# Kernel tuning notes

Measured on AMD Instinct MI355X. Metric: run time of the kernel, lower is better.

Reference implementation:

```python
import jax, jax.numpy as jnp
import numpy as np
from jax import lax

C_IN = 768      # in_channels == out_channels (required by routing_weight.view)
C_OUT = 768
E = 3           # num_experts
K = 3           # kernel_size
S = max(C_IN // 16, 16)  # squeeze_channels = 48
H = W = 120     # divisible by 3 and 5 -> adaptive pools are exact block means


def _bicubic_mat(in_size, out_size):
    """PyTorch-style bicubic (a=-0.75), align_corners=False, border-replicate."""
    a = -0.75
    def k(x):
        x = abs(x)
        if x <= 1.0:
            return (a + 2) * x**3 - (a + 3) * x**2 + 1.0
        if x < 2.0:
            return a * x**3 - 5 * a * x**2 + 8 * a * x - 4 * a
        return 0.0
    M = np.zeros((out_size, in_size), dtype=np.float32)
    scale = in_size / out_size
    for j in range(out_size):
        src = (j + 0.5) * scale - 0.5
        i0 = int(np.floor(src))
        t = src - i0
        for m in range(-1, 3):
            idx = min(max(i0 + m, 0), in_size - 1)
            M[j, idx] += k(m - t)
    return M

_M35 = jnp.asarray(_bicubic_mat(3, 5))  # (5, 3) separable interp matrix
_DN = ('NCHW', 'OIHW', 'NCHW')


def _route(x, w_pw1, w_dw1, w_dw2, w_pw2):
    b, c, h, w = x.shape
    a1 = x.mean(axis=(2, 3), keepdims=True)                       # (b,C,1,1)
    a3 = x.reshape(b, c, 3, h // 3, 3, w // 3).mean(axis=(3, 5))  # (b,C,3,3)
    a5 = x.reshape(b, c, 5, h // 5, 5, w // 5).mean(axis=(3, 5))  # (b,C,5,5)
    a3u = jnp.einsum('pi,bcij,qj->bcpq', _M35, a3, _M35)          # bicubic 3->5
    a1e = jnp.broadcast_to(a1, a5.shape)
    att = jnp.concatenate([a1e, a3u, a5], axis=1)                 # (b,3C,5,5)
    hdd = jax.nn.relu(jnp.einsum('oc,bchw->bohw', w_pw1, att))    # 1x1 conv -> (b,S,5,5)
    hdd = jax.nn.relu(lax.conv_general_dilated(hdd, w_dw1, (1, 1), 'VALID',
                                               dimension_numbers=_DN,
                                               feature_group_count=S))  # (b,S,3,3)
    hdd = jax.nn.relu(lax.conv_general_dilated(hdd, w_dw2, (1, 1), 'VALID',
                                               dimension_numbers=_DN,
                                               feature_group_count=S))  # (b,S,1,1)
    out = jnp.einsum('os,bshw->bohw', w_pw2, hdd)                 # (b,E*C,1,1)
    return jax.nn.sigmoid(out)


def setup_inputs() -> dict:
    key = jax.random.key(0)
    ks = jax.random.split(key, 6)
    return {
        'x':      jax.random.normal(ks[0], (1, C_IN, H, W), dtype=jnp.float32),
        'convs':  jax.random.normal(ks[1], (E, C_OUT, C_IN, K, K), dtype=jnp.float32) * 0.02,
        'w_pw1':  jax.random.normal(ks[2], (S, 3 * C_IN), dtype=jnp.float32) * 0.05,
        'w_dw1':  jax.random.normal(ks[3], (S, 1, 3, 3), dtype=jnp.float32) * 0.1,
        'w_dw2':  jax.random.normal(ks[4], (S, 1, 3, 3), dtype=jnp.float32) * 0.1,
        'w_pw2':  jax.random.normal(ks[5], (E * C_IN, S), dtype=jnp.float32) * 0.05,
    }


def reference(x, convs, w_pw1, w_dw1, w_dw2, w_pw2):
    # batch=1 inference path (DyResConv_Inf is only valid for b=1)
    r = _route(x, w_pw1, w_dw1, w_dw2, w_pw2)      # (1, E*C_OUT, 1, 1)
    r = r.reshape(E, C_OUT)                        # per-expert, per-out-channel gate
    w = jnp.einsum('eo,eoikl->oikl', r, convs)     # fused weight synthesis
    y = lax.conv_general_dilated(x, w, (1, 1), [(1, 1), (1, 1)],
                                 dimension_numbers=_DN)  # stride=1, pad=1
    return y
```

## Files before the change

### kernel.cpp

```cpp
#include <hip/hip_runtime.h>
#include <hip/hip_bf16.h>
#include <cstdint>
#include <cstddef>

#define C_IN 768
#define HW 120
#define WP 122
#define PIX (HW*HW)
#define PPIX (WP*WP)
#define S_CH 48
#define CCH 256
#define LSTR 257

#define OFF_POOL 0
#define OFF_HDD3 163840
#define OFF_WT   262144
#define OFF_XTP  10878976

typedef __attribute__((ext_vector_type(8))) short short8;
typedef __attribute__((ext_vector_type(4))) float floatx4;
typedef __attribute__((ext_vector_type(4))) uint uint4v;

#define AS3(p) ((__attribute__((address_space(3))) uint*)(p))
#define AS1(p) ((const __attribute__((address_space(1))) uint*)(p))

__device__ inline ushort f2bf(float f) {
  union { float f; uint i; } v; v.f = f;
  uint r = v.i + 0x7FFF + ((v.i >> 16) & 1);
  return (ushort)(r >> 16);
}

__device__ __constant__ float M35[5][3] = {
  { 1.096f, -0.096f,  0.000f },
  { 0.612f,  0.460f, -0.072f },
  { 0.000f,  1.000f,  0.000f },
  {-0.072f,  0.460f,  0.612f },
  { 0.000f, -0.096f,  1.096f },
};

__global__ __launch_bounds__(256) void k_pad_transpose(const float* __restrict__ x,
                                                       ushort* __restrict__ xTp) {
  int ph = blockIdx.x;
  int c0 = blockIdx.y * CCH;
  int tid = threadIdx.x;
  ushort* rowbase = xTp + (size_t)ph * WP * C_IN;
  if (ph == 0 || ph == WP - 1) {
    uint4v z = {0, 0, 0, 0};
    for (int i = tid; i < WP * (CCH / 8); i += 256) {
      int w = i / (CCH / 8), j = i % (CCH / 8);
      *(uint4v*)&rowbase[(size_t)w * C_IN + c0 + j * 8] = z;
    }
    return;
  }
  int h = ph - 1;
  __shared__ ushort T[HW * LSTR];
  int wave = tid >> 6, lane = tid & 63;
  for (int k = 0; k < 64; k++) {
    int cl = wave * 64 + k;
    const float* src = x + (size_t)(c0 + cl) * PIX + h * HW;
    if (lane < 60) {
      float vx = src[2 * lane], vy = src[2 * lane + 1];
      T[(2 * lane) * LSTR + cl]     = f2bf(vx);
      T[(2 * lane + 1) * LSTR + cl] = f2bf(vy);
    }
  }
  __syncthreads();
  if (tid < 128) {
    *(uint*)&rowbase[c0 + 2 * tid] = 0;
    *(uint*)&rowbase[(size_t)(WP - 1) * C_IN + c0 + 2 * tid] = 0;
  }
  for (int idx = tid; idx < HW * (CCH / 2); idx += 256) {
    int w = idx >> 7, pr = idx & 127;
    uint a = T[w * LSTR + 2 * pr];
    uint b = T[w * LSTR + 2 * pr + 1];
    *(uint*)&rowbase[(size_t)(1 + w) * C_IN + c0 + 2 * pr] = a | (b << 16);
  }
}

__global__ __launch_bounds__(256) void k_pool(const float* __restrict__ x,
                                              float* __restrict__ pooled) {
  int c = blockIdx.x;
  int tid = threadIdx.x;
  __shared__ float fine[225];
  __shared__ float s3[9], a3v[9], a5v[25];
  if (tid < 225) {
    int fr = tid / 15, fc = tid % 15;
    const float* base = x + (size_t)c * PIX + fr * 8 * HW + fc * 8;
    float s = 0.f;
#pragma unroll
    for (int r = 0; r < 8; r++) {
      floatx4 a = *(const floatx4*)(base + r * HW);
      floatx4 b = *(const floatx4*)(base + r * HW + 4);
#pragma unroll
      for (int j = 0; j < 4; j++) s += a[j] + b[j];
    }
    fine[tid] = s;
  }
  __syncthreads();
  if (tid < 9) {
    int i = tid / 3, j = tid % 3;
    float s = 0.f;
    for (int a = 0; a < 5; a++) for (int b = 0; b < 5; b++) s += fine[(i*5+a)*15 + j*5+b];
    s3[tid] = s; a3v[tid] = s / 1600.f;
  } else if (tid >= 32 && tid < 57) {
    int t = tid - 32; int p = t / 5, q = t % 5;
    float s = 0.f;
    for (int a = 0; a < 3; a++) for (int b = 0; b < 3; b++) s += fine[(p*3+a)*15 + q*3+b];
    a5v[t] = s / 576.f;
  }
  __syncthreads();
  float* out = pooled + c * 51;
  if (tid == 63) {
    float tot = 0.f;
    for (int k = 0; k < 9; k++) tot += s3[k];
    out[0] = tot / 14400.f;
  }
  if (tid < 25) {
    int p = tid / 5, q = tid % 5;
    float s = 0.f;
    for (int i = 0; i < 3; i++) for (int j = 0; j < 3; j++)
      s += M35[p][i] * M35[q][j] * a3v[i*3+j];
    out[1 + tid] = s;
    out[26 + tid] = a5v[tid];
  }
}

__global__ __launch_bounds__(256) void k_route(const float* __restrict__ pooled,
                                               const float* __restrict__ w_pw1,
                                               const float* __restrict__ w_dw1,
                                               const float* __restrict__ w_dw2,
                                               float* __restrict__ hdd3) {
  int s = blockIdx.x;
  int tid = threadIdx.x;
  __shared__ float red[26][256];
  float acc[25]; float accw1 = 0.f;
#pragma unroll
  for (int q = 0; q < 25; q++) acc[q] = 0.f;
  for (int c = tid; c < C_IN; c += 256) {
    const float* pl = pooled + c * 51;
    float w1 = w_pw1[(size_t)s * 3 * C_IN + c];
    float w2 = w_pw1[(size_t)s * 3 * C_IN + C_IN + c];
    float w3 = w_pw1[(size_t)s * 3 * C_IN + 2 * C_IN + c];
    accw1 += w1 * pl[0];
#pragma unroll
    for (int q = 0; q < 25; q++) acc[q] += w2 * pl[1 + q] + w3 * pl[26 + q];
  }
#pragma unroll
  for (int q = 0; q < 25; q++) red[q][tid] = acc[q];
  red[25][tid] = accw1;
  for (int st = 128; st; st >>= 1) {
    __syncthreads();
    if (tid < st)
      for (int q = 0; q < 26; q++) red[q][tid] += red[q][tid + st];
  }
  __syncthreads();
  if (tid == 0) {
    float hdd[5][5];
    for (int p = 0; p < 5; p++) for (int q = 0; q < 5; q++) {
      float v = red[p*5+q][0] + red[25][0];
      hdd[p][q] = v > 0.f ? v : 0.f;
    }
    float wd1[9], wd2[9];
    for (int i = 0; i < 9; i++) { wd1[i] = w_dw1[s*9 + i]; wd2[i] = w_dw2[s*9 + i]; }
    float h2[3][3];
    for (int i = 0; i < 3; i++) for (int j = 0; j < 3; j++) {
      float v = 0.f;
      for (int u = 0; u < 3; u++) for (int vv = 0; vv < 3; vv++) v += wd1[u*3+vv] * hdd[i+u][j+vv];
      h2[i][j] = v > 0.f ? v : 0.f;
    }
    float v = 0.f;
    for (int u = 0; u < 3; u++) for (int vv = 0; vv < 3; vv++) v += wd2[u*3+vv] * h2[u][vv];
    hdd3[s] = v > 0.f ? v : 0.f;
  }
}

__global__ __launch_bounds__(256) void k_wt(const float* __restrict__ convs,
                                            const float* __restrict__ w_pw2,
                                            const float* __restrict__ hdd3,
                                            ushort* __restrict__ wt) {
  int o = blockIdx.x;
  int tid = threadIdx.x;
  __shared__ float g[3];
  __shared__ __align__(16) ushort st[9 * C_IN];
  if (tid < 3) {
    float v = 0.f;
    for (int s = 0; s < S_CH; s++)
      v += w_pw2[((size_t)tid * C_IN + o) * S_CH + s] * hdd3[s];
    g[tid] = 1.f / (1.f + __expf(-v));
  }
  __syncthreads();
  float g0 = g[0], g1 = g[1], g2 = g[2];
  const float* c0p = convs + (size_t)o * 6912;
  const float* c1p = convs + (size_t)(C_IN + o) * 6912;
  const float* c2p = convs + (size_t)(2 * C_IN + o) * 6912;
  for (int i = tid * 4; i < 6912; i += 1024) {
    floatx4 a = *(const floatx4*)(c0p + i);
    floatx4 b = *(const floatx4*)(c1p + i);
    floatx4 c = *(const floatx4*)(c2p + i);
#pragma unroll
    for (int j = 0; j < 4; j++) {
      int idx = i + j;
      int cch = idx / 9, tap = idx - cch * 9;
      st[tap * C_IN + cch] = f2bf(g0 * a[j] + g1 * b[j] + g2 * c[j]);
    }
  }
  __syncthreads();
  for (int i = tid; i < 864; i += 256) {
    int tap = i / 96, j = i - tap * 96;
    *(uint4v*)&wt[((size_t)(tap * C_IN + o)) * C_IN + j * 8] =
        *(const uint4v*)&st[tap * C_IN + j * 8];
  }
}

__global__ __launch_bounds__(128) void k_conv(const ushort* __restrict__ xTp,
                                              const ushort* __restrict__ wt,
                                              float* __restrict__ y) {
  __shared__ __align__(16) ushort Aun[2][768 * 8];
  __shared__ __align__(16) ushort Bt[2][256 * 8];
  int tid = threadIdx.x;
  int lane = tid & 63;
  int quad = lane >> 4, l15 = lane & 15;
  int wave = tid >> 6;

  int bid = blockIdx.x;
  int wg = (bid & 7) * 180 + (bid >> 3);
  int n_t = wg / 120, m_t = wg - n_t * 120;
  int h0 = (m_t >> 3) << 3;
  int w0 = (m_t & 7) << 4;
  int n0 = n_t << 6;

  uint a_off[6];
#pragma unroll
  for (int r = 0; r < 6; r++) {
    int t = r * 128 + tid;
    int p = t >> 2; if (p > 179) p = 179;
    int sl = (t & 3) ^ ((p >> 1) & 3);
    int pr = p / 18, pc = p - pr * 18;
    int pix = (h0 + pr) * WP + (w0 + pc);
    if (pix > PPIX - 1) pix = PPIX - 1;
    a_off[r] = (uint)pix * C_IN + sl * 8;
  }
  uint b_off[2];
#pragma unroll
  for (int r = 0; r < 2; r++) {
    int t = r * 128 + tid;
    int n = t >> 2;
    int sl = (t & 3) ^ ((n >> 1) & 3);
    b_off[r] = (uint)(n0 + n) * C_IN + sl * 8;
  }
  int b_rd[4];
#pragma unroll
  for (int nt = 0; nt < 4; nt++) {
    int n = nt * 16 + l15;
    b_rd[nt] = n * 32 + ((quad ^ ((n >> 1) & 3)) << 3);
  }
  int amh = wave * 4;
  int P0[4];
#pragma unroll
  for (int mt = 0; mt < 4; mt++) P0[mt] = (amh + mt) * 18 + l15;

  auto stageA = [&](int ncc, int na) {
#pragma unroll
    for (int r = 0; r < 6; r++)
      __builtin_amdgcn_global_load_lds(AS1(xTp + a_off[r] + ncc * 32),
                                       AS3(&Aun[na][(r * 128 + wave * 64) * 8]), 16, 0, 0);
  };
  auto stageB = [&](int ncc, int ntap, int nb) {
    const ushort* wb = wt + (size_t)ntap * C_IN * C_IN + ncc * 32;
#pragma unroll
    for (int r = 0; r < 2; r++)
      __builtin_amdgcn_global_load_lds(AS1(wb + b_off[r]),
                                       AS3(&Bt[nb][(r * 128 + wave * 64) * 8]), 16, 0, 0);
  };

  floatx4 acc[4][4];
#pragma unroll
  for (int i = 0; i < 4; i++)
#pragma unroll
    for (int j = 0; j < 4; j++) acc[i][j] = (floatx4){0.f, 0.f, 0.f, 0.f};

  stageA(0, 0);
  stageB(0, 0, 0);
  __syncthreads();

  int pb = 0;
  for (int cc = 0; cc < 24; cc++) {
    int pa = cc & 1;
#pragma unroll
    for (int tap = 0; tap < 9; tap++) {
      const int kh = tap / 3, kw = tap % 3;
      if (tap < 8) {
        stageB(cc, tap + 1, pb ^ 1);
      } else if (cc < 23) {
        stageB(cc + 1, 0, pb ^ 1);
        stageA(cc + 1, pa ^ 1);
      }
      short8 bfr[4], af[4];
#pragma unroll
      for (int nt = 0; nt < 4; nt++) bfr[nt] = *(const short8*)&Bt[pb][b_rd[nt]];
#pragma unroll
      for (int mt = 0; mt < 4; mt++) {
        int p = P0[mt] + kh * 18 + kw;
        int idx = p * 32 + ((quad ^ ((p >> 1) & 3)) << 3);
        af[mt] = *(const short8*)&Aun[pa][idx];
      }
#pragma unroll
      for (int mt = 0; mt < 4; mt++)
#pragma unroll
        for (int nt = 0; nt < 4; nt++)
          acc[mt][nt] = __builtin_amdgcn_mfma_f32_16x16x32_bf16(af[mt], bfr[nt], acc[mt][nt], 0, 0, 0);
      __syncthreads();
      pb ^= 1;
    }
  }

#pragma unroll
  for (int mt = 0; mt < 4; mt++) {
    int h = h0 + wave * 4 + mt;
    int wbase = w0 + quad * 4;
    if (wbase < HW) {
#pragma unroll
      for (int nt = 0; nt < 4; nt++) {
        int n = n0 + nt * 16 + l15;
        *(floatx4*)&y[(size_t)n * PIX + h * HW + wbase] = acc[mt][nt];
      }
    }
  }
}

extern "C" void kernel_launch(void* const* d_in, const int* in_sizes, int n_in,
                              void* d_out, int out_size, void* d_ws, size_t ws_size,
                              hipStream_t stream) {
  const float* x     = (const float*)d_in[0];
  const float* convs = (const float*)d_in[1];
  const float* w_pw1 = (const float*)d_in[2];
  const float* w_dw1 = (const float*)d_in[3];
  const float* w_dw2 = (const float*)d_in[4];
  const float* w_pw2 = (const float*)d_in[5];
  float* y = (float*)d_out;
  char* ws = (char*)d_ws;
  float*  pooled = (float*)(ws + OFF_POOL);
  float*  hdd3   = (float*)(ws + OFF_HDD3);
  ushort* wt     = (ushort*)(ws + OFF_WT);
  ushort* xTp    = (ushort*)(ws + OFF_XTP);

  hipLaunchKernelGGL(k_pad_transpose, dim3(122, 3), dim3(256), 0, stream, x, xTp);
  hipLaunchKernelGGL(k_pool,          dim3(768),    dim3(256), 0, stream, x, pooled);
  hipLaunchKernelGGL(k_route,         dim3(48),     dim3(256), 0, stream, pooled, w_pw1, w_dw1, w_dw2, hdd3);
  hipLaunchKernelGGL(k_wt,            dim3(768),    dim3(256), 0, stream, convs, w_pw2, hdd3, wt);
  hipLaunchKernelGGL(k_conv,          dim3(1440),   dim3(128), 0, stream, xTp, wt, y);
}
```

Baseline: 410.9 us.

## Enlarge conv tile to 192x256 with 8 waves and 4-slot B pipeline

The implicit-GEMM conv kernel moves from 128-thread blocks with 128x64 tiles to 512-thread blocks covering 12 rows by 16 columns and 256 output channels, split over 8 waves in a 2x4 arrangement. The K-step doubles to 64 channels and is split into two 32-wide halves. B tiles rotate through four LDS slots and A is double-buffered, with explicit vmcnt waits, raw s_barrier and setprio around the MFMA blocks. The larger tile raises weight and activation reuse per byte loaded and lowers barrier overhead. In exchange it uses much more LDS and registers, and only 240 blocks are launched, which may leave some CUs idle.

New measurement: 329.2 us. 1.25x faster.

```diff
diff --git a/kernel.cpp b/kernel.cpp
--- a/kernel.cpp
+++ b/kernel.cpp
@@ -212,116 +212,166 @@
   }
 }
 
-__global__ __launch_bounds__(128) void k_conv(const ushort* __restrict__ xTp,
-                                              const ushort* __restrict__ wt,
-                                              float* __restrict__ y) {
-  __shared__ __align__(16) ushort Aun[2][768 * 8];
-  __shared__ __align__(16) ushort Bt[2][256 * 8];
+#define WAITV(N) asm volatile("s_waitcnt vmcnt(" #N ")" ::: "memory")
+#define FENCE()  asm volatile("" ::: "memory")
+
+#define PHASE(WSTMT, KS, RSLOT, PAv, KH, KW, STAGES) do {                      \
+    WSTMT;                                                                     \
+    short8 bfr[4], af[6];                                                      \
+    _Pragma("unroll")                                                          \
+    for (int nt = 0; nt < 4; nt++)                                             \
+      bfr[nt] = *(const short8*)&Bt[RSLOT][b_rd[nt]];                          \
+    _Pragma("unroll")                                                          \
+    for (int mt = 0; mt < 6; mt++) {                                           \
+      int u_ = P0[mt] + ((KH) * 18 + (KW));                                    \
+      int idx_ = u_ * 32 + ((quad ^ ((u_ >> 1) & 3)) << 3);                    \
+      af[mt] = *(const short8*)&Aun[PAv][KS][idx_];                            \
+    }                                                                          \
+    STAGES;                                                                    \
+    FENCE();                                                                   \
+    __builtin_amdgcn_s_barrier();                                              \
+    __builtin_amdgcn_sched_barrier(0);                                         \
+    __builtin_amdgcn_s_setprio(1);                                             \
+    _Pragma("unroll")                                                          \
+    for (int mt = 0; mt < 6; mt++)                                             \
+      _Pragma("unroll")                                                        \
+      for (int nt = 0; nt < 4; nt++)                                           \
+        acc[mt][nt] = __builtin_amdgcn_mfma_f32_16x16x32_bf16(af[mt], bfr[nt], \
+                                                              acc[mt][nt], 0, 0, 0); \
+    __builtin_amdgcn_s_setprio(0);                                             \
+  } while (0)
+
+#define CCB(ccv, P, PAv) do { const int cc_ = (ccv);                               \
+    PHASE(;,        0, ((0+P)&3),  PAv, 0,0, { SB(1, cc_, 1, ((3+P)&3)); });        \
+    PHASE(WAITV(0), 1, ((1+P)&3),  PAv, 0,0, { SB(2, cc_, 0, ((0+P)&3)); });        \
+    PHASE(;,        0, ((2+P)&3),  PAv, 0,1, { SB(2, cc_, 1, ((5+P)&3)); });        \
+    PHASE(WAITV(0), 1, ((3+P)&3),  PAv, 0,1, { SB(3, cc_, 0, ((2+P)&3)); });        \
+    PHASE(;,        0, ((4+P)&3),  PAv, 0,2, { SB(3, cc_, 1, ((7+P)&3)); });        \
+    PHASE(WAITV(0), 1, ((5+P)&3),  PAv, 0,2, { SB(4, cc_, 0, ((4+P)&3)); });        \
+    PHASE(;,        0, ((6+P)&3),  PAv, 1,0, { SB(4, cc_, 1, ((9+P)&3)); });        \
+    PHASE(WAITV(0), 1, ((7+P)&3),  PAv, 1,0, { SB(5, cc_, 0, ((6+P)&3)); });        \
+    PHASE(;,        0, ((8+P)&3),  PAv, 1,1, { SB(5, cc_, 1, ((11+P)&3)); SA(cc_+1, (PAv)^1, 0); }); \
+    PHASE(WAITV(1), 1, ((9+P)&3),  PAv, 1,1, { SB(6, cc_, 0, ((8+P)&3));  SA(cc_+1, (PAv)^1, 1); }); \
+    PHASE(;,        0, ((10+P)&3), PAv, 1,2, { SB(6, cc_, 1, ((13+P)&3)); SA(cc_+1, (PAv)^1, 2); }); \
+    PHASE(WAITV(1), 1, ((11+P)&3), PAv, 1,2, { SB(7, cc_, 0, ((10+P)&3)); SA(cc_+1, (PAv)^1, 3); }); \
+    PHASE(;,        0, ((12+P)&3), PAv, 2,0, { SB(7, cc_, 1, ((15+P)&3)); });       \
+    PHASE(WAITV(0), 1, ((13+P)&3), PAv, 2,0, { SB(8, cc_, 0, ((12+P)&3)); });       \
+    PHASE(;,        0, ((14+P)&3), PAv, 2,1, { SB(8, cc_, 1, ((17+P)&3)); });       \
+    PHASE(WAITV(0), 1, ((15+P)&3), PAv, 2,1, { SB(0, cc_+1, 0, ((14+P)&3)); });     \
+    PHASE(;,        0, ((16+P)&3), PAv, 2,2, { SB(0, cc_+1, 1, ((19+P)&3)); });     \
+    PHASE(WAITV(0), 1, ((17+P)&3), PAv, 2,2, { SB(1, cc_+1, 0, ((16+P)&3)); });     \
+  } while (0)
+
+#define CCB11() do { const int cc_ = 11;                                           \
+    PHASE(;,        0, ((0+2)&3),  1, 0,0, { SB(1, cc_, 1, ((3+2)&3)); });          \
+    PHASE(WAITV(0), 1, ((1+2)&3),  1, 0,0, { SB(2, cc_, 0, ((0+2)&3)); });          \
+    PHASE(;,        0, ((2+2)&3),  1, 0,1, { SB(2, cc_, 1, ((5+2)&3)); });          \
+    PHASE(WAITV(0), 1, ((3+2)&3),  1, 0,1, { SB(3, cc_, 0, ((2+2)&3)); });          \
+    PHASE(;,        0, ((4+2)&3),  1, 0,2, { SB(3, cc_, 1, ((7+2)&3)); });          \
+    PHASE(WAITV(0), 1, ((5+2)&3),  1, 0,2, { SB(4, cc_, 0, ((4+2)&3)); });          \
+    PHASE(;,        0, ((6+2)&3),  1, 1,0, { SB(4, cc_, 1, ((9+2)&3)); });          \
+    PHASE(WAITV(0), 1, ((7+2)&3),  1, 1,0, { SB(5, cc_, 0, ((6+2)&3)); });          \
+    PHASE(;,        0, ((8+2)&3),  1, 1,1, { SB(5, cc_, 1, ((11+2)&3)); });         \
+    PHASE(WAITV(0), 1, ((9+2)&3),  1, 1,1, { SB(6, cc_, 0, ((8+2)&3)); });          \
+    PHASE(;,        0, ((10+2)&3), 1, 1,2, { SB(6, cc_, 1, ((13+2)&3)); });         \
+    PHASE(WAITV(0), 1, ((11+2)&3), 1, 1,2, { SB(7, cc_, 0, ((10+2)&3)); });         \
+    PHASE(;,        0, ((12+2)&3), 1, 2,0, { SB(7, cc_, 1, ((15+2)&3)); });         \
+    PHASE(WAITV(0), 1, ((13+2)&3), 1, 2,0, { SB(8, cc_, 0, ((12+2)&3)); });         \
+    PHASE(;,        0, ((14+2)&3), 1, 2,1, { SB(8, cc_, 1, ((17+2)&3)); });         \
+    PHASE(WAITV(0), 1, ((15+2)&3), 1, 2,1, { ; });                                  \
+    PHASE(;,        0, ((16+2)&3), 1, 2,2, { ; });                                  \
+    PHASE(;,        1, ((17+2)&3), 1, 2,2, { ; });                                  \
+  } while (0)
+
+__global__ __launch_bounds__(512, 2) void k_conv(const ushort* __restrict__ xTp,
+                                                 const ushort* __restrict__ wt,
+                                                 float* __restrict__ y) {
+  __shared__ __align__(16) ushort Aun[2][2][8192];
+  __shared__ __align__(16) ushort Bt[4][8192];
   int tid = threadIdx.x;
   int lane = tid & 63;
   int quad = lane >> 4, l15 = lane & 15;
   int wave = tid >> 6;
+  int wm = wave >> 2, wn = wave & 3;
 
   int bid = blockIdx.x;
-  int wg = (bid & 7) * 180 + (bid >> 3);
-  int n_t = wg / 120, m_t = wg - n_t * 120;
-  int h0 = (m_t >> 3) << 3;
+  int wg = (bid & 7) * 30 + (bid >> 3);
+  int n_t = wg / 80, m_t = wg - n_t * 80;
+  int h0 = (m_t >> 3) * 12;
   int w0 = (m_t & 7) << 4;
-  int n0 = n_t << 6;
-
-  uint a_off[6];
-#pragma unroll
-  for (int r = 0; r < 6; r++) {
-    int t = r * 128 + tid;
-    int p = t >> 2; if (p > 179) p = 179;
-    int sl = (t & 3) ^ ((p >> 1) & 3);
-    int pr = p / 18, pc = p - pr * 18;
-    int pix = (h0 + pr) * WP + (w0 + pc);
+  int n0 = n_t << 8;
+
+  size_t a_off[4];
+#pragma unroll
+  for (int r = 0; r < 4; r++) {
+    int t = r * 512 + tid;
+    int ks = t >> 10;
+    int u = (t >> 2) & 255; if (u > 251) u = 251;
+    int sl = (t & 3) ^ ((u >> 1) & 3);
+    int ur = u / 18, uc = u - ur * 18;
+    int pix = (h0 + ur) * WP + (w0 + uc);
     if (pix > PPIX - 1) pix = PPIX - 1;
-    a_off[r] = (uint)pix * C_IN + sl * 8;
-  }
-  uint b_off[2];
+    a_off[r] = (size_t)pix * C_IN + ks * 32 + sl * 8;
+  }
+  size_t b_off[2];
 #pragma unroll
   for (int r = 0; r < 2; r++) {
-    int t = r * 128 + tid;
+    int t = r * 512 + tid;
     int n = t >> 2;
     int sl = (t & 3) ^ ((n >> 1) & 3);
-    b_off[r] = (uint)(n0 + n) * C_IN + sl * 8;
+    b_off[r] = (size_t)(n0 + n) * C_IN + sl * 8;
   }
   int b_rd[4];
 #pragma unroll
   for (int nt = 0; nt < 4; nt++) {
-    int n = nt * 16 + l15;
+    int n = wn * 64 + nt * 16 + l15;
     b_rd[nt] = n * 32 + ((quad ^ ((n >> 1) & 3)) << 3);
   }
-  int amh = wave * 4;
-  int P0[4];
-#pragma unroll
-  for (int mt = 0; mt < 4; mt++) P0[mt] = (amh + mt) * 18 + l15;
-
-  auto stageA = [&](int ncc, int na) {
-#pragma unroll
-    for (int r = 0; r < 6; r++)
-      __builtin_amdgcn_global_load_lds(AS1(xTp + a_off[r] + ncc * 32),
-                                       AS3(&Aun[na][(r * 128 + wave * 64) * 8]), 16, 0, 0);
+  int P0[6];
+#pragma unroll
+  for (int mt = 0; mt < 6; mt++) P0[mt] = (wm * 6 + mt) * 18 + l15;
+
+  auto SB = [&](int gtap, int gcc, int ks, int slot) {
+    const ushort* src = wt + (size_t)gtap * (C_IN * C_IN) + gcc * 64 + ks * 32;
+#pragma unroll
+    for (int r = 0; r < 2; r++)
+      __builtin_amdgcn_global_load_lds(AS1(src + b_off[r]),
+                                       AS3(&Bt[slot][r * 4096 + wave * 512]), 16, 0, 0);
   };
-  auto stageB = [&](int ncc, int ntap, int nb) {
-    const ushort* wb = wt + (size_t)ntap * C_IN * C_IN + ncc * 32;
-#pragma unroll
-    for (int r = 0; r < 2; r++)
-      __builtin_amdgcn_global_load_lds(AS1(wb + b_off[r]),
-                                       AS3(&Bt[nb][(r * 128 + wave * 64) * 8]), 16, 0, 0);
+  auto SA = [&](int gcc, int pa, int r) {
+    __builtin_amdgcn_global_load_lds(AS1(xTp + a_off[r] + gcc * 64),
+                                     AS3(&Aun[pa][0][0] + r * 4096 + wave * 512), 16, 0, 0);
   };
 
-  floatx4 acc[4][4];
-#pragma unroll
-  for (int i = 0; i < 4; i++)
+  floatx4 acc[6][4];
+#pragma unroll
+  for (int i = 0; i < 6; i++)
 #pragma unroll
     for (int j = 0; j < 4; j++) acc[i][j] = (floatx4){0.f, 0.f, 0.f, 0.f};
 
-  stageA(0, 0);
-  stageB(0, 0, 0);
-  __syncthreads();
-
-  int pb = 0;
-  for (int cc = 0; cc < 24; cc++) {
-    int pa = cc & 1;
-#pragma unroll
-    for (int tap = 0; tap < 9; tap++) {
-      const int kh = tap / 3, kw = tap % 3;
-      if (tap < 8) {
-        stageB(cc, tap + 1, pb ^ 1);
-      } else if (cc < 23) {
-        stageB(cc + 1, 0, pb ^ 1);
-        stageA(cc + 1, pa ^ 1);
-      }
-      short8 bfr[4], af[4];
-#pragma unroll
-      for (int nt = 0; nt < 4; nt++) bfr[nt] = *(const short8*)&Bt[pb][b_rd[nt]];
-#pragma unroll
-      for (int mt = 0; mt < 4; mt++) {
-        int p = P0[mt] + kh * 18 + kw;
-        int idx = p * 32 + ((quad ^ ((p >> 1) & 3)) << 3);
-        af[mt] = *(const short8*)&Aun[pa][idx];
-      }
-#pragma unroll
-      for (int mt = 0; mt < 4; mt++)
-#pragma unroll
-        for (int nt = 0; nt < 4; nt++)
-          acc[mt][nt] = __builtin_amdgcn_mfma_f32_16x16x32_bf16(af[mt], bfr[nt], acc[mt][nt], 0, 0, 0);
-      __syncthreads();
-      pb ^= 1;
-    }
-  }
-
-#pragma unroll
-  for (int mt = 0; mt < 4; mt++) {
-    int h = h0 + wave * 4 + mt;
+  SB(0, 0, 0, 0);
+  SB(0, 0, 1, 1);
+  SA(0, 0, 0); SA(0, 0, 1); SA(0, 0, 2); SA(0, 0, 3);
+  SB(1, 0, 0, 2);
+  WAITV(2);
+  FENCE();
+  __builtin_amdgcn_s_barrier();
+
+  for (int cc = 0; cc < 10; cc += 2) {
+    CCB(cc,     0, 0);
+    CCB(cc + 1, 2, 1);
+  }
+  CCB(10, 0, 0);
+  CCB11();
+
+#pragma unroll
+  for (int mt = 0; mt < 6; mt++) {
+    int h = h0 + wm * 6 + mt;
     int wbase = w0 + quad * 4;
     if (wbase < HW) {
 #pragma unroll
       for (int nt = 0; nt < 4; nt++) {
-        int n = n0 + nt * 16 + l15;
+        int n = n0 + wn * 64 + nt * 16 + l15;
         *(floatx4*)&y[(size_t)n * PIX + h * HW + wbase] = acc[mt][nt];
       }
     }
@@ -348,5 +398,5 @@
   hipLaunchKernelGGL(k_pool,          dim3(768),    dim3(256), 0, stream, x, pooled);
   hipLaunchKernelGGL(k_route,         dim3(48),     dim3(256), 0, stream, pooled, w_pw1, w_dw1, w_dw2, hdd3);
   hipLaunchKernelGGL(k_wt,            dim3(768),    dim3(256), 0, stream, convs, w_pw2, hdd3, wt);
-  hipLaunchKernelGGL(k_conv,          dim3(1440),   dim3(128), 0, stream, xTp, wt, y);
-}
+  hipLaunchKernelGGL(k_conv,          dim3(240),    dim3(512), 0, stream, xTp, wt, y);
+}
```
